# Performance work log

Hardware: AMD Instinct MI355X
Metric: run time of the kernel (lower is better)

The kernel has to match this reference:

```python
import jax, jax.numpy as jnp
import numpy as np

N_NODES = 100_000
N_EDGES = 1_600_000
D_IN, D_HID, N_CLASSES = 128, 128, 40


def setup_inputs() -> dict:
    key = jax.random.key(0)
    ks = jax.random.split(key, 8)
    x = jax.random.normal(ks[0], (N_NODES, D_IN), dtype=jnp.float32)
    edge_index = jax.random.randint(ks[1], (2, N_EDGES), 0, N_NODES, dtype=jnp.int64)
    dims = [(D_IN, D_HID), (D_HID, D_HID), (D_HID, N_CLASSES)]
    inp = {"x": x, "edge_index": edge_index}
    for i, (di, do) in enumerate(dims):
        s = 1.0 / np.sqrt(di)
        inp[f"W_l{i}"] = jax.random.normal(ks[2 + 2 * i], (di, do), dtype=jnp.float32) * s
        inp[f"W_r{i}"] = jax.random.normal(ks[3 + 2 * i], (di, do), dtype=jnp.float32) * s
        inp[f"b{i}"] = jnp.zeros((do,), dtype=jnp.float32)
    return inp


def _sage_conv(x, src, dst, deg_inv, W_l, W_r, b):
    # gather messages from source nodes, mean-aggregate at target nodes
    msg = x[src]                                        # [E, d_in]
    aggr = jax.ops.segment_sum(msg, dst, num_segments=N_NODES) * deg_inv  # [N, d_in]
    return aggr @ W_l + b + x @ W_r                     # [N, d_out]


def reference(x, edge_index, W_l0, W_r0, b0, W_l1, W_r1, b1, W_l2, W_r2, b2):
    src, dst = edge_index[0], edge_index[1]
    deg = jax.ops.segment_sum(jnp.ones((N_EDGES,), x.dtype), dst, num_segments=N_NODES)
    deg_inv = (1.0 / jnp.maximum(deg, 1.0))[:, None]    # [N, 1]

    h = _sage_conv(x, src, dst, deg_inv, W_l0, W_r0, b0)
    h = jax.nn.relu(h)  # dropout p=0.3 is identity in eval mode
    h = _sage_conv(h, src, dst, deg_inv, W_l1, W_r1, b1)
    h = jax.nn.relu(h)
    h = _sage_conv(h, src, dst, deg_inv, W_l2, W_r2, b2)
    return jax.nn.log_softmax(h, axis=1)
```

## Files before the change

kernel.cpp:

```cpp
#include <hip/hip_runtime.h>
#include <math.h>

#define THREADS 256
#define BSHIFT 8
#define BSIZE 256
#define NEB 512

typedef short short8 __attribute__((ext_vector_type(8)));
typedef float f32x4 __attribute__((ext_vector_type(4)));

__device__ __forceinline__ unsigned short f2bf(float f) {
  unsigned u = __builtin_bit_cast(unsigned, f);
  return (unsigned short)((u + 0x7FFFu + ((u >> 16) & 1u)) >> 16);
}
__device__ __forceinline__ float bflo(unsigned u) {
  return __builtin_bit_cast(float, u << 16);
}
__device__ __forceinline__ float bfhi(unsigned u) {
  return __builtin_bit_cast(float, u & 0xFFFF0000u);
}
__device__ __forceinline__ unsigned pack2(float x, float y) {
  return (unsigned)f2bf(x) | ((unsigned)f2bf(y) << 16);
}

__device__ __forceinline__ void acc8(float* a, uint4 u) {
  a[0] += bflo(u.x); a[1] += bfhi(u.x);
  a[2] += bflo(u.y); a[3] += bfhi(u.y);
  a[4] += bflo(u.z); a[5] += bfhi(u.z);
  a[6] += bflo(u.w); a[7] += bfhi(u.w);
}

__device__ __forceinline__ void gemm128_body(
    const short8 xf[4], const short8 xg[4],
    const unsigned short* __restrict__ Wswz, const float* __restrict__ bias,
    unsigned short* __restrict__ outL, unsigned short* __restrict__ outR,
    int M, int lane,
    unsigned short (*lt)[16][136], int rb0) {
  int quad = lane >> 4, n16 = lane & 15;
#pragma unroll
  for (int ct = 0; ct < 8; ++ct) {
    f32x4 accA = {0.f, 0.f, 0.f, 0.f};
    f32x4 accB = {0.f, 0.f, 0.f, 0.f};
    const unsigned short* wp = Wswz + (size_t)(ct * 64 + lane) * 8;
#pragma unroll
    for (int ks = 0; ks < 4; ++ks) {
      short8 wf = *(const short8*)(wp + ks * 8192);
      accA = __builtin_amdgcn_mfma_f32_16x16x32_bf16(wf, xf[ks], accA, 0, 0, 0);
      accB = __builtin_amdgcn_mfma_f32_16x16x32_bf16(wf, xg[ks], accB, 0, 0, 0);
    }
    int ch = ct * 16 + quad * 4;
    ushort4 oA, oB;
    oA.x = f2bf(accA[0]); oA.y = f2bf(accA[1]); oA.z = f2bf(accA[2]); oA.w = f2bf(accA[3]);
    oB.x = f2bf(accB[0]); oB.y = f2bf(accB[1]); oB.z = f2bf(accB[2]); oB.w = f2bf(accB[3]);
    *(ushort4*)&lt[0][n16][ch] = oA;
    *(ushort4*)&lt[1][n16][ch] = oB;
  }
#pragma unroll
  for (int r = 0; r < 4; ++r) {
    int nd = r * 4 + (lane >> 4);
    int ic = (lane & 15) * 8;
    uint4 vA = *(const uint4*)&lt[0][nd][ic];
    uint4 vB = *(const uint4*)&lt[1][nd][ic];
    if (rb0 + nd < M)      *(uint4*)(outL + ((size_t)(rb0 + nd)) * 128 + ic) = vA;
    if (rb0 + 64 + nd < M) *(uint4*)(outL + ((size_t)(rb0 + 64 + nd)) * 128 + ic) = vB;
  }
#pragma unroll
  for (int ct = 8; ct < 16; ++ct) {
    f32x4 accA = {0.f, 0.f, 0.f, 0.f};
    f32x4 accB = {0.f, 0.f, 0.f, 0.f};
    const unsigned short* wp = Wswz + (size_t)(ct * 64 + lane) * 8;
#pragma unroll
    for (int ks = 0; ks < 4; ++ks) {
      short8 wf = *(const short8*)(wp + ks * 8192);
      accA = __builtin_amdgcn_mfma_f32_16x16x32_bf16(wf, xf[ks], accA, 0, 0, 0);
      accB = __builtin_amdgcn_mfma_f32_16x16x32_bf16(wf, xg[ks], accB, 0, 0, 0);
    }
    int ch = (ct - 8) * 16 + quad * 4;
    float4 bv = *(const float4*)(bias + ch);
    ushort4 oA, oB;
    oA.x = f2bf(accA[0] + bv.x); oA.y = f2bf(accA[1] + bv.y);
    oA.z = f2bf(accA[2] + bv.z); oA.w = f2bf(accA[3] + bv.w);
    oB.x = f2bf(accB[0] + bv.x); oB.y = f2bf(accB[1] + bv.y);
    oB.z = f2bf(accB[2] + bv.z); oB.w = f2bf(accB[3] + bv.w);
    *(ushort4*)&lt[0][n16][ch] = oA;
    *(ushort4*)&lt[1][n16][ch] = oB;
  }
#pragma unroll
  for (int r = 0; r < 4; ++r) {
    int nd = r * 4 + (lane >> 4);
    int ic = (lane & 15) * 8;
    uint4 vA = *(const uint4*)&lt[0][nd][ic];
    uint4 vB = *(const uint4*)&lt[1][nd][ic];
    if (rb0 + nd < M)      *(uint4*)(outR + ((size_t)(rb0 + nd)) * 128 + ic) = vA;
    if (rb0 + 64 + nd < M) *(uint4*)(outR + ((size_t)(rb0 + 64 + nd)) * 128 + ic) = vB;
  }
}

__global__ __launch_bounds__(256) void k_phase0(
    const int* __restrict__ dst, int* __restrict__ cnt_bm, int E, int chunk, int nbk,
    const float* __restrict__ Wl0, const float* __restrict__ Wr0,
    const float* __restrict__ Wl1, const float* __restrict__ Wr1,
    const float* __restrict__ Wl2, const float* __restrict__ Wr2,
    unsigned short* __restrict__ out0, unsigned short* __restrict__ out1,
    unsigned short* __restrict__ out2) {
  int b = blockIdx.x, t = threadIdx.x;
  if (b < NEB) {
    __shared__ int h[1024];
    for (int i = t; i < nbk; i += 256) h[i] = 0;
    __syncthreads();
    int e0 = b * chunk, e1 = min(e0 + chunk, E);
    for (int e = e0 + t; e < e1; e += 256) atomicAdd(&h[dst[e] >> BSHIFT], 1);
    __syncthreads();
    for (int i = t; i < nbk; i += 256) cnt_bm[(size_t)b * nbk + i] = h[i];
    return;
  }
  int wb = b - NEB;
  if (wb < 256) {
    const float* Wl = (wb < 128) ? Wl0 : Wl1;
    const float* Wr = (wb < 128) ? Wr0 : Wr1;
    unsigned short* out = (wb < 128) ? out0 : out1;
    int idx = (wb & 127) * 256 + t;
    int j = idx & 7, lane = (idx >> 3) & 63, ct = (idx >> 9) & 15, ks = idx >> 13;
    int k = ks * 32 + (lane >> 4) * 8 + j;
    int c = ct * 16 + (lane & 15);
    float v = (c < 128) ? Wl[k * 128 + c] : Wr[k * 128 + (c - 128)];
    out[idx] = f2bf(v);
  } else {
    int idx = (wb - 256) * 256 + t;
    int j = idx & 7, lane = (idx >> 3) & 63;
    int tile = idx >> 9;
    int ct = tile % 5, ks = tile / 5;
    int k = ks * 32 + (lane >> 4) * 8 + j;
    int c = ct * 16 + (lane & 15);
    float v = (c < 40) ? Wl2[k * 40 + c] : ((c < 80) ? Wr2[k * 40 + (c - 40)] : 0.f);
    out2[idx] = f2bf(v);
  }
}

__global__ __launch_bounds__(256) void k_phase1(
    const int* __restrict__ cnt_bm, int* __restrict__ locoff_tm,
    int* __restrict__ bktot, int nbk,
    const float* __restrict__ X, const unsigned short* __restrict__ Wswz,
    const float* __restrict__ bias,
    unsigned short* __restrict__ outL, unsigned short* __restrict__ outR, int M) {
  __shared__ int sh[256];
  __shared__ __align__(16) unsigned short lt[4][2][16][136];
  int t = threadIdx.x;
  if (blockIdx.x < (unsigned)nbk) {
    int g = blockIdx.x;
    int c0 = cnt_bm[(size_t)(2 * t) * nbk + g];
    int c1 = cnt_bm[(size_t)(2 * t + 1) * nbk + g];
    int s = c0 + c1;
    sh[t] = s;
    __syncthreads();
    for (int off = 1; off < 256; off <<= 1) {
      int v = (t >= off) ? sh[t - off] : 0;
      __syncthreads();
      if (t >= off) sh[t] += v;
      __syncthreads();
    }
    int excl = sh[t] - s;
    ((int2*)(locoff_tm + (size_t)g * NEB))[t] = make_int2(excl, excl + c0);
    if (t == 255) bktot[g] = sh[255];
    return;
  }
  int gb = blockIdx.x - nbk;
  int wave = t >> 6, lane = t & 63;
  int quad = lane >> 4, n16 = lane & 15;
  int rowA = gb * 128 + wave * 16 + n16;
  int rA = min(rowA, M - 1), rB = min(rowA + 64, M - 1);

  short8 xf[4], xg[4];
  const float* xpA = X + (size_t)rA * 128 + quad * 8;
  const float* xpB = X + (size_t)rB * 128 + quad * 8;
#pragma unroll
  for (int ks = 0; ks < 4; ++ks) {
    float4 a0 = *(const float4*)(xpA + ks * 32);
    float4 a1 = *(const float4*)(xpA + ks * 32 + 4);
    float4 b0 = *(const float4*)(xpB + ks * 32);
    float4 b1 = *(const float4*)(xpB + ks * 32 + 4);
    short8 f, g;
    f[0] = (short)f2bf(a0.x); f[1] = (short)f2bf(a0.y);
    f[2] = (short)f2bf(a0.z); f[3] = (short)f2bf(a0.w);
    f[4] = (short)f2bf(a1.x); f[5] = (short)f2bf(a1.y);
    f[6] = (short)f2bf(a1.z); f[7] = (short)f2bf(a1.w);
    g[0] = (short)f2bf(b0.x); g[1] = (short)f2bf(b0.y);
    g[2] = (short)f2bf(b0.z); g[3] = (short)f2bf(b0.w);
    g[4] = (short)f2bf(b1.x); g[5] = (short)f2bf(b1.y);
    g[6] = (short)f2bf(b1.z); g[7] = (short)f2bf(b1.w);
    xf[ks] = f;
    xg[ks] = g;
  }
  gemm128_body(xf, xg, Wswz, bias, outL, outR, M, lane,
               lt[wave], gb * 128 + wave * 16);
}

__global__ __launch_bounds__(256) void k_eplace2(
    const int* __restrict__ src, const int* __restrict__ dst,
    const int* __restrict__ bktot, const int* __restrict__ locoff_tm,
    int* __restrict__ bedge, int* __restrict__ bucket_base,
    int* __restrict__ row_ptr,
    int E, int chunk, int nbk, int N) {
  __shared__ int lptr[1024];
  __shared__ int psum[256];
  int blk = blockIdx.x, t = threadIdx.x;
  int v0 = (2 * t < nbk) ? bktot[2 * t] : 0;
  int v1 = (2 * t + 1 < nbk) ? bktot[2 * t + 1] : 0;
  int s = v0 + v1;
  psum[t] = s;
  __syncthreads();
  for (int off = 1; off < 256; off <<= 1) {
    int v = (t >= off) ? psum[t - off] : 0;
    __syncthreads();
    if (t >= off) psum[t] += v;
    __syncthreads();
  }
  int excl = psum[t] - s;
  if (2 * t < nbk)
    lptr[2 * t] = excl + locoff_tm[(size_t)(2 * t) * NEB + blk];
  if (2 * t + 1 < nbk)
    lptr[2 * t + 1] = excl + v0 + locoff_tm[(size_t)(2 * t + 1) * NEB + blk];
  if (blk == 0) {
    if (2 * t < nbk)     bucket_base[2 * t] = excl;
    if (2 * t + 1 < nbk) bucket_base[2 * t + 1] = excl + v0;
    if (t == 0) { bucket_base[nbk] = E; row_ptr[N] = E; }
  }
  __syncthreads();
  int e0 = blk * chunk, e1 = min(e0 + chunk, E);
  for (int e = e0 + t; e < e1; e += 256) {
    int d = dst[e];
    int bkt = d >> BSHIFT;
    int p = atomicAdd(&lptr[bkt], 1);
    bedge[p] = (src[e] << 8) | (d & (BSIZE - 1));
  }
}

__global__ __launch_bounds__(256) void k_bcsr2(const int* __restrict__ bedge,
                                               const int* __restrict__ bucket_base,
                                               int* __restrict__ row_ptr,
                                               int* __restrict__ col, int N) {
  int g = blockIdx.x, t = threadIdx.x;
  int beg = bucket_base[g], end = bucket_base[g + 1];
  __shared__ int deg[BSIZE];
  __shared__ int sh[BSIZE];
  __shared__ int cur[BSIZE];
  deg[t] = 0;
  __syncthreads();
  for (int i = beg + t; i < end; i += 256)
    atomicAdd(&deg[bedge[i] & (BSIZE - 1)], 1);
  __syncthreads();
  int s = deg[t];
  sh[t] = s;
  __syncthreads();
  for (int off = 1; off < 256; off <<= 1) {
    int v = (t >= off) ? sh[t - off] : 0;
    __syncthreads();
    if (t >= off) sh[t] += v;
    __syncthreads();
  }
  int ex = beg + sh[t] - s;
  int node = g * BSIZE + t;
  if (node < N) row_ptr[node] = ex;
  cur[t] = ex;
  __syncthreads();
  for (int i = beg + t; i < end; i += 256) {
    int ed = bedge[i];
    int p = atomicAdd(&cur[ed & (BSIZE - 1)], 1);
    col[p] = ed >> 8;
  }
}

__global__ __launch_bounds__(256) void gemm128_mfma(
    const unsigned short* __restrict__ Xb, const unsigned short* __restrict__ Wswz,
    const float* __restrict__ bias,
    unsigned short* __restrict__ outL, unsigned short* __restrict__ outR, int M) {
  __shared__ __align__(16) unsigned short lt[4][2][16][136];
  int wave = threadIdx.x >> 6, lane = threadIdx.x & 63;
  int quad = lane >> 4, n16 = lane & 15;
  int rowA = blockIdx.x * 128 + wave * 16 + n16;
  int rA = min(rowA, M - 1), rB = min(rowA + 64, M - 1);

  short8 xf[4], xg[4];
  const unsigned short* xpA = Xb + (size_t)rA * 128 + quad * 8;
  const unsigned short* xpB = Xb + (size_t)rB * 128 + quad * 8;
#pragma unroll
  for (int ks = 0; ks < 4; ++ks) {
    xf[ks] = *(const short8*)(xpA + ks * 32);
    xg[ks] = *(const short8*)(xpB + ks * 32);
  }
  gemm128_body(xf, xg, Wswz, bias, outL, outR, M, lane,
               lt[wave], blockIdx.x * 128 + wave * 16);
}

__global__ __launch_bounds__(256) void gemm40_mfma(
    const unsigned short* __restrict__ Xb, const unsigned short* __restrict__ Wswz,
    const float* __restrict__ bias,
    unsigned short* __restrict__ tlb, float* __restrict__ tr, int M) {
  int wave = threadIdx.x >> 6, lane = threadIdx.x & 63;
  int quad = lane >> 4, n16 = lane & 15;
  int row = blockIdx.x * 64 + wave * 16 + n16;
  int row_ld = min(row, M - 1);
  bool ok = row < M;

  short8 xf[4];
  const unsigned short* xp = Xb + (size_t)row_ld * 128 + quad * 8;
#pragma unroll
  for (int ks = 0; ks < 4; ++ks) xf[ks] = *(const short8*)(xp + ks * 32);

#pragma unroll
  for (int ct = 0; ct < 5; ++ct) {
    f32x4 acc = {0.f, 0.f, 0.f, 0.f};
    const unsigned short* wp = Wswz + (size_t)(ct * 64 + lane) * 8;
#pragma unroll
    for (int ks = 0; ks < 4; ++ks) {
      short8 wf = *(const short8*)(wp + (size_t)ks * 5 * 64 * 8);
      acc = __builtin_amdgcn_mfma_f32_16x16x32_bf16(wf, xf[ks], acc, 0, 0, 0);
    }
    int cglob = ct * 16 + quad * 4;
    if (!ok) continue;
    if (cglob < 40) {
      ushort4 o;
      o.x = f2bf(acc[0]); o.y = f2bf(acc[1]); o.z = f2bf(acc[2]); o.w = f2bf(acc[3]);
      *(ushort4*)(tlb + (size_t)row * 40 + cglob) = o;
    } else {
      int c = cglob - 40;
      float4 bv = *(const float4*)(bias + c);
      float4 o;
      o.x = acc[0] + bv.x; o.y = acc[1] + bv.y;
      o.z = acc[2] + bv.z; o.w = acc[3] + bv.w;
      *(float4*)(tr + (size_t)row * 40 + c) = o;
    }
  }
}

__global__ __launch_bounds__(256) void agg128b(
    const unsigned short* __restrict__ xl, const unsigned short* __restrict__ xr,
    const int* __restrict__ row_ptr, const int* __restrict__ col,
    unsigned short* __restrict__ h, int Nn) {
  int wave = threadIdx.x >> 6;
  int lane = threadIdx.x & 63;
  int pair = lane >> 5;
  int l32 = lane & 31;
  int n = blockIdx.x * 4 + wave;
  if (n >= Nn) return;
  int beg = row_ptr[n], end = row_ptr[n + 1];
  int deg = end - beg;
  const uint2* xlq = (const uint2*)xl;
  float a0x = 0.f, a0y = 0.f, a0z = 0.f, a0w = 0.f;
  float a1x = 0.f, a1y = 0.f, a1z = 0.f, a1w = 0.f;
  float a2x = 0.f, a2y = 0.f, a2z = 0.f, a2w = 0.f;
  float a3x = 0.f, a3y = 0.f, a3z = 0.f, a3w = 0.f;
  int e = beg + pair;
  for (int it = deg >> 3; it > 0; --it, e += 8) {
    uint2 u0 = xlq[(size_t)col[e]     * 32 + l32];
    uint2 u1 = xlq[(size_t)col[e + 2] * 32 + l32];
    uint2 u2 = xlq[(size_t)col[e + 4] * 32 + l32];
    uint2 u3 = xlq[(size_t)col[e + 6] * 32 + l32];
    a0x += bflo(u0.x); a0y += bfhi(u0.x); a0z += bflo(u0.y); a0w += bfhi(u0.y);
    a1x += bflo(u1.x); a1y += bfhi(u1.x); a1z += bflo(u1.y); a1w += bfhi(u1.y);
    a2x += bflo(u2.x); a2y += bfhi(u2.x); a2z += bflo(u2.y); a2w += bfhi(u2.y);
    a3x += bflo(u3.x); a3y += bfhi(u3.x); a3z += bflo(u3.y); a3w += bfhi(u3.y);
  }
  for (; e < end; e += 2) {
    uint2 u = xlq[(size_t)col[e] * 32 + l32];
    a0x += bflo(u.x); a0y += bfhi(u.x); a0z += bflo(u.y); a0w += bfhi(u.y);
  }
  float ax = (a0x + a1x) + (a2x + a3x);
  float ay = (a0y + a1y) + (a2y + a3y);
  float az = (a0z + a1z) + (a2z + a3z);
  float aw = (a0w + a1w) + (a2w + a3w);
  ax += __shfl_xor(ax, 32);
  ay += __shfl_xor(ay, 32);
  az += __shfl_xor(az, 32);
  aw += __shfl_xor(aw, 32);
  if (pair == 0) {
    float di = 1.0f / (float)max(deg, 1);
    uint2 r = ((const uint2*)xr)[(size_t)n * 32 + l32];
    float ox = fmaxf(fmaf(ax, di, bflo(r.x)), 0.f);
    float oy = fmaxf(fmaf(ay, di, bfhi(r.x)), 0.f);
    float oz = fmaxf(fmaf(az, di, bflo(r.y)), 0.f);
    float ow = fmaxf(fmaf(aw, di, bfhi(r.y)), 0.f);
    uint2 o;
    o.x = pack2(ox, oy);
    o.y = pack2(oz, ow);
    ((uint2*)h)[(size_t)n * 32 + l32] = o;
  }
}

__global__ __launch_bounds__(256) void agg40_lsm(
    const unsigned short* __restrict__ tlb, const float* __restrict__ tr,
    const int* __restrict__ row_ptr, const int* __restrict__ col,
    float* __restrict__ out, int Nn) {
  int wave = threadIdx.x >> 6;
  int lane = threadIdx.x & 63;
  int ew = lane >> 3;
  int l8 = lane & 7;
  int n = blockIdx.x * 4 + wave;
  if (n >= Nn) return;
  int beg = row_ptr[n], end = row_ptr[n + 1];
  int deg = end - beg;
  const uint4* tlq = (const uint4*)tlb;
  float a0[8], a1[8];
#pragma unroll
  for (int j = 0; j < 8; ++j) { a0[j] = 0.f; a1[j] = 0.f; }
  int rounds = (deg + 15) >> 4;
  if (rounds > 0) {
    int end1 = end - 1;
    int e = beg + ew;
    int c0 = col[min(e, end1)];
    int c1 = col[min(e + 8, end1)];
    for (int it = rounds - 1; it > 0; --it) {
      uint4 u0 = tlq[(size_t)c0 * 5 + l8];
      uint4 u1 = tlq[(size_t)c1 * 5 + l8];
      int en = e + 16;
      int cn0 = col[min(en, end1)];
      int cn1 = col[min(en + 8, end1)];
      acc8(a0, u0); acc8(a1, u1);
      c0 = cn0; c1 = cn1; e = en;
    }
    uint4 u0 = tlq[(size_t)c0 * 5 + l8];
    uint4 u1 = tlq[(size_t)c1 * 5 + l8];
    uint4 z = make_uint4(0u, 0u, 0u, 0u);
    if (e >= end) u0 = z;
    if (e + 8 >= end) u1 = z;
    acc8(a0, u0); acc8(a1, u1);
  }
  float v[8];
#pragma unroll
  for (int j = 0; j < 8; ++j) {
    float t = a0[j] + a1[j];
    t += __shfl_xor(t, 32);
    t += __shfl_xor(t, 16);
    t += __shfl_xor(t, 8);
    v[j] = t;
  }
  bool valid = l8 < 5;
  float di = 1.0f / (float)max(deg, 1);
  float4 r0 = valid ? *(const float4*)(tr + (size_t)n * 40 + 8 * l8)
                    : make_float4(0.f, 0.f, 0.f, 0.f);
  float4 r1 = valid ? *(const float4*)(tr + (size_t)n * 40 + 8 * l8 + 4)
                    : make_float4(0.f, 0.f, 0.f, 0.f);
  float rb[8] = {r0.x, r0.y, r0.z, r0.w, r1.x, r1.y, r1.z, r1.w};
  float vv[8];
#pragma unroll
  for (int j = 0; j < 8; ++j) vv[j] = valid ? fmaf(v[j], di, rb[j]) : -INFINITY;
  float m = vv[0];
#pragma unroll
  for (int j = 1; j < 8; ++j) m = fmaxf(m, vv[j]);
#pragma unroll
  for (int off = 4; off; off >>= 1) m = fmaxf(m, __shfl_xor(m, off));
  float ex = 0.f;
  if (valid) {
#pragma unroll
    for (int j = 0; j < 8; ++j) ex += expf(vv[j] - m);
  }
  float ssum = ex;
#pragma unroll
  for (int off = 4; off; off >>= 1) ssum += __shfl_xor(ssum, off);
  float lg = logf(ssum);
  if (ew == 0 && valid) {
    float4 o0, o1;
    o0.x = (vv[0] - m) - lg; o0.y = (vv[1] - m) - lg;
    o0.z = (vv[2] - m) - lg; o0.w = (vv[3] - m) - lg;
    o1.x = (vv[4] - m) - lg; o1.y = (vv[5] - m) - lg;
    o1.z = (vv[6] - m) - lg; o1.w = (vv[7] - m) - lg;
    *(float4*)(out + (size_t)n * 40 + 8 * l8) = o0;
    *(float4*)(out + (size_t)n * 40 + 8 * l8 + 4) = o1;
  }
}


extern "C" void kernel_launch(void* const* d_in, const int* in_sizes, int n_in,
                              void* d_out, int out_size, void* d_ws, size_t ws_size,
                              hipStream_t stream) {
  const float* x   = (const float*)d_in[0];
  const int*   ei  = (const int*)d_in[1];
  const float* Wl0 = (const float*)d_in[2];
  const float* Wr0 = (const float*)d_in[3];
  const float* b0  = (const float*)d_in[4];
  const float* Wl1 = (const float*)d_in[5];
  const float* Wr1 = (const float*)d_in[6];
  const float* b1  = (const float*)d_in[7];
  const float* Wl2 = (const float*)d_in[8];
  const float* Wr2 = (const float*)d_in[9];
  const float* b2  = (const float*)d_in[10];

  int N = in_sizes[0] / 128;
  int E = in_sizes[1] / 2;
  const int* src = ei;
  const int* dst = ei + E;
  int nbk = (N + BSIZE - 1) / BSIZE;
  int chunk = (E + NEB - 1) / NEB;

  char* ws = (char*)d_ws;
  size_t off = 0;
  auto alloc = [&](size_t bytes) -> void* {
    void* p = ws + off;
    off += (bytes + 255) & ~(size_t)255;
    return p;
  };
  unsigned short* gA  = (unsigned short*)alloc((size_t)N * 128 * 2);
  unsigned short* gB  = (unsigned short*)alloc((size_t)N * 128 * 2);
  unsigned short* hC  = (unsigned short*)alloc((size_t)N * 128 * 2);
  unsigned short* tlb = (unsigned short*)alloc((size_t)N * 40 * 2);
  float* tr           = (float*)alloc((size_t)N * 40 * 4);
  int* row_ptr  = (int*)alloc((size_t)(N + 1) * 4);
  int* col      = (int*)alloc((size_t)E * 4);
  int* bedge    = (int*)alloc((size_t)E * 4);
  int* cnt_bm   = (int*)alloc((size_t)NEB * nbk * 4);
  int* locoff   = (int*)alloc((size_t)nbk * NEB * 4);
  int* bktot    = (int*)alloc((size_t)nbk * 4);
  int* bbase    = (int*)alloc((size_t)(nbk + 1) * 4);
  unsigned short* wswz0 = (unsigned short*)alloc(32768 * 2);
  unsigned short* wswz1 = (unsigned short*)alloc(32768 * 2);
  unsigned short* wswz2 = (unsigned short*)alloc(10240 * 2);
  (void)ws_size; (void)n_in; (void)out_size;

  int gg128 = (N + 127) / 128;
  int gg = (N + 63) / 64;
  int nb = (N + 3) / 4;

  k_phase0<<<NEB + 296, 256, 0, stream>>>(dst, cnt_bm, E, chunk, nbk,
                                          Wl0, Wr0, Wl1, Wr1, Wl2, Wr2,
                                          wswz0, wswz1, wswz2);
  k_phase1<<<nbk + gg128, 256, 0, stream>>>(cnt_bm, locoff, bktot, nbk,
                                            x, wswz0, b0, gA, gB, N);
  k_eplace2<<<NEB, 256, 0, stream>>>(src, dst, bktot, locoff, bedge, bbase,
                                     row_ptr, E, chunk, nbk, N);
  k_bcsr2<<<nbk, 256, 0, stream>>>(bedge, bbase, row_ptr, col, N);

  agg128b<<<nb, 256, 0, stream>>>(gA, gB, row_ptr, col, hC, N);
  gemm128_mfma<<<gg128, 256, 0, stream>>>(hC, wswz1, b1, gA, gB, N);
  agg128b<<<nb, 256, 0, stream>>>(gA, gB, row_ptr, col, hC, N);
  gemm40_mfma<<<gg, 256, 0, stream>>>(hC, wswz2, b2, tlb, tr, N);
  agg40_lsm<<<nb, 256, 0, stream>>>(tlb, tr, row_ptr, col, (float*)d_out, N);
}
```

Measured before the change: 400.2 us.

## Fuse neighbor aggregation with following MFMA GEMM via shared-memory staging

Merges each 128-wide aggregation kernel with the next layer's GEMM. A block aggregates 128 (or 64) nodes into LDS, synchronizes, then runs the MFMA GEMM straight from LDS. This removes the hC intermediate write and re-read and cuts two kernel launches. The cost is that the GEMM waves sit idle behind a block barrier while aggregation finishes, and aggregation now runs as 8 or 4 waves per block covering 16 nodes each sequentially, which may reduce latency hiding for the irregular gathers. Buffers are double-buffered (gA2/gB2) and tlb/tr alias gA.

```diff
diff --git a/kernel.cpp b/kernel.cpp
--- a/kernel.cpp
+++ b/kernel.cpp
@@ -28,6 +28,53 @@
   a[2] += bflo(u.y); a[3] += bfhi(u.y);
   a[4] += bflo(u.z); a[5] += bfhi(u.z);
   a[6] += bflo(u.w); a[7] += bfhi(u.w);
+}
+
+__device__ __forceinline__ void agg_node(
+    const uint2* __restrict__ xlq, const unsigned short* __restrict__ xr,
+    const int* __restrict__ row_ptr, const int* __restrict__ col,
+    int n, int pair, int l32, unsigned short* abrow) {
+  int beg = row_ptr[n], end = row_ptr[n + 1];
+  int deg = end - beg;
+  float a0x = 0.f, a0y = 0.f, a0z = 0.f, a0w = 0.f;
+  float a1x = 0.f, a1y = 0.f, a1z = 0.f, a1w = 0.f;
+  float a2x = 0.f, a2y = 0.f, a2z = 0.f, a2w = 0.f;
+  float a3x = 0.f, a3y = 0.f, a3z = 0.f, a3w = 0.f;
+  int e = beg + pair;
+  for (int it = deg >> 3; it > 0; --it, e += 8) {
+    uint2 u0 = xlq[(size_t)col[e]     * 32 + l32];
+    uint2 u1 = xlq[(size_t)col[e + 2] * 32 + l32];
+    uint2 u2 = xlq[(size_t)col[e + 4] * 32 + l32];
+    uint2 u3 = xlq[(size_t)col[e + 6] * 32 + l32];
+    a0x += bflo(u0.x); a0y += bfhi(u0.x); a0z += bflo(u0.y); a0w += bfhi(u0.y);
+    a1x += bflo(u1.x); a1y += bfhi(u1.x); a1z += bflo(u1.y); a1w += bfhi(u1.y);
+    a2x += bflo(u2.x); a2y += bfhi(u2.x); a2z += bflo(u2.y); a2w += bfhi(u2.y);
+    a3x += bflo(u3.x); a3y += bfhi(u3.x); a3z += bflo(u3.y); a3w += bfhi(u3.y);
+  }
+  for (; e < end; e += 2) {
+    uint2 u = xlq[(size_t)col[e] * 32 + l32];
+    a0x += bflo(u.x); a0y += bfhi(u.x); a0z += bflo(u.y); a0w += bfhi(u.y);
+  }
+  float ax = (a0x + a1x) + (a2x + a3x);
+  float ay = (a0y + a1y) + (a2y + a3y);
+  float az = (a0z + a1z) + (a2z + a3z);
+  float aw = (a0w + a1w) + (a2w + a3w);
+  ax += __shfl_xor(ax, 32);
+  ay += __shfl_xor(ay, 32);
+  az += __shfl_xor(az, 32);
+  aw += __shfl_xor(aw, 32);
+  if (pair == 0) {
+    float di = 1.0f / (float)max(deg, 1);
+    uint2 r = ((const uint2*)xr)[(size_t)n * 32 + l32];
+    float ox = fmaxf(fmaf(ax, di, bflo(r.x)), 0.f);
+    float oy = fmaxf(fmaf(ay, di, bfhi(r.x)), 0.f);
+    float oz = fmaxf(fmaf(az, di, bflo(r.y)), 0.f);
+    float ow = fmaxf(fmaf(aw, di, bfhi(r.y)), 0.f);
+    uint2 o;
+    o.x = pack2(ox, oy);
+    o.y = pack2(oz, ow);
+    *(uint2*)(abrow + l32 * 4) = o;
+  }
 }
 
 __device__ __forceinline__ void gemm128_body(
@@ -270,43 +317,65 @@
   }
 }
 
-__global__ __launch_bounds__(256) void gemm128_mfma(
-    const unsigned short* __restrict__ Xb, const unsigned short* __restrict__ Wswz,
-    const float* __restrict__ bias,
-    unsigned short* __restrict__ outL, unsigned short* __restrict__ outR, int M) {
+__global__ __launch_bounds__(512) void k_aggemm128(
+    const unsigned short* __restrict__ xl, const unsigned short* __restrict__ xr,
+    const int* __restrict__ row_ptr, const int* __restrict__ col,
+    const unsigned short* __restrict__ Wswz, const float* __restrict__ bias,
+    unsigned short* __restrict__ outL, unsigned short* __restrict__ outR, int Nn) {
+  __shared__ __align__(16) unsigned short ab[128][132];
   __shared__ __align__(16) unsigned short lt[4][2][16][136];
   int wave = threadIdx.x >> 6, lane = threadIdx.x & 63;
+  int pair = lane >> 5, l32 = lane & 31;
+  int nb0 = blockIdx.x * 128;
+  const uint2* xlq = (const uint2*)xl;
+#pragma unroll 1
+  for (int i = 0; i < 16; ++i) {
+    int nl = wave * 16 + i;
+    int n = nb0 + nl;
+    if (n >= Nn) break;
+    agg_node(xlq, xr, row_ptr, col, n, pair, l32, &ab[nl][0]);
+  }
+  __syncthreads();
+  if (wave < 4) {
+    int quad = lane >> 4, n16 = lane & 15;
+    int rowAl = wave * 16 + n16;
+    short8 xf[4], xg[4];
+#pragma unroll
+    for (int ks = 0; ks < 4; ++ks) {
+      xf[ks] = *(const short8*)&ab[rowAl][quad * 8 + ks * 32];
+      xg[ks] = *(const short8*)&ab[rowAl + 64][quad * 8 + ks * 32];
+    }
+    gemm128_body(xf, xg, Wswz, bias, outL, outR, Nn, lane,
+                 lt[wave], nb0 + wave * 16);
+  }
+}
+
+__global__ __launch_bounds__(256) void k_aggemm40(
+    const unsigned short* __restrict__ xl, const unsigned short* __restrict__ xr,
+    const int* __restrict__ row_ptr, const int* __restrict__ col,
+    const unsigned short* __restrict__ Wswz, const float* __restrict__ bias,
+    unsigned short* __restrict__ tlb, float* __restrict__ tr, int Nn) {
+  __shared__ __align__(16) unsigned short ab[64][132];
+  int wave = threadIdx.x >> 6, lane = threadIdx.x & 63;
+  int pair = lane >> 5, l32 = lane & 31;
+  int nb0 = blockIdx.x * 64;
+  const uint2* xlq = (const uint2*)xl;
+#pragma unroll 1
+  for (int i = 0; i < 16; ++i) {
+    int nl = wave * 16 + i;
+    int n = nb0 + nl;
+    if (n >= Nn) break;
+    agg_node(xlq, xr, row_ptr, col, n, pair, l32, &ab[nl][0]);
+  }
+  __syncthreads();
   int quad = lane >> 4, n16 = lane & 15;
-  int rowA = blockIdx.x * 128 + wave * 16 + n16;
-  int rA = min(rowA, M - 1), rB = min(rowA + 64, M - 1);
-
-  short8 xf[4], xg[4];
-  const unsigned short* xpA = Xb + (size_t)rA * 128 + quad * 8;
-  const unsigned short* xpB = Xb + (size_t)rB * 128 + quad * 8;
-#pragma unroll
-  for (int ks = 0; ks < 4; ++ks) {
-    xf[ks] = *(const short8*)(xpA + ks * 32);
-    xg[ks] = *(const short8*)(xpB + ks * 32);
-  }
-  gemm128_body(xf, xg, Wswz, bias, outL, outR, M, lane,
-               lt[wave], blockIdx.x * 128 + wave * 16);
-}
-
-__global__ __launch_bounds__(256) void gemm40_mfma(
-    const unsigned short* __restrict__ Xb, const unsigned short* __restrict__ Wswz,
-    const float* __restrict__ bias,
-    unsigned short* __restrict__ tlb, float* __restrict__ tr, int M) {
-  int wave = threadIdx.x >> 6, lane = threadIdx.x & 63;
-  int quad = lane >> 4, n16 = lane & 15;
-  int row = blockIdx.x * 64 + wave * 16 + n16;
-  int row_ld = min(row, M - 1);
-  bool ok = row < M;
-
+  int rl = wave * 16 + n16;
+  int row = nb0 + rl;
+  bool ok = row < Nn;
   short8 xf[4];
-  const unsigned short* xp = Xb + (size_t)row_ld * 128 + quad * 8;
-#pragma unroll
-  for (int ks = 0; ks < 4; ++ks) xf[ks] = *(const short8*)(xp + ks * 32);
-
+#pragma unroll
+  for (int ks = 0; ks < 4; ++ks)
+    xf[ks] = *(const short8*)&ab[rl][quad * 8 + ks * 32];
 #pragma unroll
   for (int ct = 0; ct < 5; ++ct) {
     f32x4 acc = {0.f, 0.f, 0.f, 0.f};
@@ -330,60 +399,6 @@
       o.z = acc[2] + bv.z; o.w = acc[3] + bv.w;
       *(float4*)(tr + (size_t)row * 40 + c) = o;
     }
-  }
-}
-
-__global__ __launch_bounds__(256) void agg128b(
-    const unsigned short* __restrict__ xl, const unsigned short* __restrict__ xr,
-    const int* __restrict__ row_ptr, const int* __restrict__ col,
-    unsigned short* __restrict__ h, int Nn) {
-  int wave = threadIdx.x >> 6;
-  int lane = threadIdx.x & 63;
-  int pair = lane >> 5;
-  int l32 = lane & 31;
-  int n = blockIdx.x * 4 + wave;
-  if (n >= Nn) return;
-  int beg = row_ptr[n], end = row_ptr[n + 1];
-  int deg = end - beg;
-  const uint2* xlq = (const uint2*)xl;
-  float a0x = 0.f, a0y = 0.f, a0z = 0.f, a0w = 0.f;
-  float a1x = 0.f, a1y = 0.f, a1z = 0.f, a1w = 0.f;
-  float a2x = 0.f, a2y = 0.f, a2z = 0.f, a2w = 0.f;
-  float a3x = 0.f, a3y = 0.f, a3z = 0.f, a3w = 0.f;
-  int e = beg + pair;
-  for (int it = deg >> 3; it > 0; --it, e += 8) {
-    uint2 u0 = xlq[(size_t)col[e]     * 32 + l32];
-    uint2 u1 = xlq[(size_t)col[e + 2] * 32 + l32];
-    uint2 u2 = xlq[(size_t)col[e + 4] * 32 + l32];
-    uint2 u3 = xlq[(size_t)col[e + 6] * 32 + l32];
-    a0x += bflo(u0.x); a0y += bfhi(u0.x); a0z += bflo(u0.y); a0w += bfhi(u0.y);
-    a1x += bflo(u1.x); a1y += bfhi(u1.x); a1z += bflo(u1.y); a1w += bfhi(u1.y);
-    a2x += bflo(u2.x); a2y += bfhi(u2.x); a2z += bflo(u2.y); a2w += bfhi(u2.y);
-    a3x += bflo(u3.x); a3y += bfhi(u3.x); a3z += bflo(u3.y); a3w += bfhi(u3.y);
-  }
-  for (; e < end; e += 2) {
-    uint2 u = xlq[(size_t)col[e] * 32 + l32];
-    a0x += bflo(u.x); a0y += bfhi(u.x); a0z += bflo(u.y); a0w += bfhi(u.y);
-  }
-  float ax = (a0x + a1x) + (a2x + a3x);
-  float ay = (a0y + a1y) + (a2y + a3y);
-  float az = (a0z + a1z) + (a2z + a3z);
-  float aw = (a0w + a1w) + (a2w + a3w);
-  ax += __shfl_xor(ax, 32);
-  ay += __shfl_xor(ay, 32);
-  az += __shfl_xor(az, 32);
-  aw += __shfl_xor(aw, 32);
-  if (pair == 0) {
-    float di = 1.0f / (float)max(deg, 1);
-    uint2 r = ((const uint2*)xr)[(size_t)n * 32 + l32];
-    float ox = fmaxf(fmaf(ax, di, bflo(r.x)), 0.f);
-    float oy = fmaxf(fmaf(ay, di, bfhi(r.x)), 0.f);
-    float oz = fmaxf(fmaf(az, di, bflo(r.y)), 0.f);
-    float ow = fmaxf(fmaf(aw, di, bfhi(r.y)), 0.f);
-    uint2 o;
-    o.x = pack2(ox, oy);
-    o.y = pack2(oz, ow);
-    ((uint2*)h)[(size_t)n * 32 + l32] = o;
   }
 }
 
@@ -501,9 +516,8 @@
   };
   unsigned short* gA  = (unsigned short*)alloc((size_t)N * 128 * 2);
   unsigned short* gB  = (unsigned short*)alloc((size_t)N * 128 * 2);
-  unsigned short* hC  = (unsigned short*)alloc((size_t)N * 128 * 2);
-  unsigned short* tlb = (unsigned short*)alloc((size_t)N * 40 * 2);
-  float* tr           = (float*)alloc((size_t)N * 40 * 4);
+  unsigned short* gA2 = (unsigned short*)alloc((size_t)N * 128 * 2);
+  unsigned short* gB2 = (unsigned short*)alloc((size_t)N * 128 * 2);
   int* row_ptr  = (int*)alloc((size_t)(N + 1) * 4);
   int* col      = (int*)alloc((size_t)E * 4);
   int* bedge    = (int*)alloc((size_t)E * 4);
@@ -514,10 +528,11 @@
   unsigned short* wswz0 = (unsigned short*)alloc(32768 * 2);
   unsigned short* wswz1 = (unsigned short*)alloc(32768 * 2);
   unsigned short* wswz2 = (unsigned short*)alloc(10240 * 2);
+  unsigned short* tlb = gA;
+  float* tr = (float*)((char*)gA + (((size_t)N * 40 * 2 + 255) & ~(size_t)255));
   (void)ws_size; (void)n_in; (void)out_size;
 
   int gg128 = (N + 127) / 128;
-  int gg = (N + 63) / 64;
   int nb = (N + 3) / 4;
 
   k_phase0<<<NEB + 296, 256, 0, stream>>>(dst, cnt_bm, E, chunk, nbk,
@@ -529,9 +544,9 @@
                                      row_ptr, E, chunk, nbk, N);
   k_bcsr2<<<nbk, 256, 0, stream>>>(bedge, bbase, row_ptr, col, N);
 
-  agg128b<<<nb, 256, 0, stream>>>(gA, gB, row_ptr, col, hC, N);
-  gemm128_mfma<<<gg128, 256, 0, stream>>>(hC, wswz1, b1, gA, gB, N);
-  agg128b<<<nb, 256, 0, stream>>>(gA, gB, row_ptr, col, hC, N);
-  gemm40_mfma<<<gg, 256, 0, stream>>>(hC, wswz2, b2, tlb, tr, N);
+  k_aggemm128<<<gg128, 512, 0, stream>>>(gA, gB, row_ptr, col,
+                                         wswz1, b1, gA2, gB2, N);
+  k_aggemm40<<<(N + 63) / 64, 256, 0, stream>>>(gA2, gB2, row_ptr, col,
+                                                wswz2, b2, tlb, tr, N);
   agg40_lsm<<<nb, 256, 0, stream>>>(tlb, tr, row_ptr, col, (float*)d_out, N);
 }
```

After: 443.2 us. +10.7%, slower.

## Fuse layer-2 aggregation with the 40-class GEMM through shared memory

Applied to the files above, without the earlier changes.

The second 128-wide aggregation and the final 128x80 MFMA GEMM now run in one kernel. Each block aggregates 64 nodes into a shared-memory tile and then multiplies it against the swizzled weights, so the hC round trip to global memory and one launch go away. The tlb/tr buffers now alias hC to save workspace. The LDS row padding for gemm128 also changes from 136 to 132. The cost is lower occupancy and less latency hiding, because each wave walks 16 nodes serially before the GEMM, and degree imbalance now stalls the barrier.

```diff
diff --git a/kernel.cpp b/kernel.cpp
--- a/kernel.cpp
+++ b/kernel.cpp
@@ -30,12 +30,59 @@
   a[6] += bflo(u.w); a[7] += bfhi(u.w);
 }
 
+__device__ __forceinline__ void agg_node(
+    const uint2* __restrict__ xlq, const unsigned short* __restrict__ xr,
+    const int* __restrict__ row_ptr, const int* __restrict__ col,
+    int n, int pair, int l32, unsigned short* abrow) {
+  int beg = row_ptr[n], end = row_ptr[n + 1];
+  int deg = end - beg;
+  float a0x = 0.f, a0y = 0.f, a0z = 0.f, a0w = 0.f;
+  float a1x = 0.f, a1y = 0.f, a1z = 0.f, a1w = 0.f;
+  float a2x = 0.f, a2y = 0.f, a2z = 0.f, a2w = 0.f;
+  float a3x = 0.f, a3y = 0.f, a3z = 0.f, a3w = 0.f;
+  int e = beg + pair;
+  for (int it = deg >> 3; it > 0; --it, e += 8) {
+    uint2 u0 = xlq[(size_t)col[e]     * 32 + l32];
+    uint2 u1 = xlq[(size_t)col[e + 2] * 32 + l32];
+    uint2 u2 = xlq[(size_t)col[e + 4] * 32 + l32];
+    uint2 u3 = xlq[(size_t)col[e + 6] * 32 + l32];
+    a0x += bflo(u0.x); a0y += bfhi(u0.x); a0z += bflo(u0.y); a0w += bfhi(u0.y);
+    a1x += bflo(u1.x); a1y += bfhi(u1.x); a1z += bflo(u1.y); a1w += bfhi(u1.y);
+    a2x += bflo(u2.x); a2y += bfhi(u2.x); a2z += bflo(u2.y); a2w += bfhi(u2.y);
+    a3x += bflo(u3.x); a3y += bfhi(u3.x); a3z += bflo(u3.y); a3w += bfhi(u3.y);
+  }
+  for (; e < end; e += 2) {
+    uint2 u = xlq[(size_t)col[e] * 32 + l32];
+    a0x += bflo(u.x); a0y += bfhi(u.x); a0z += bflo(u.y); a0w += bfhi(u.y);
+  }
+  float ax = (a0x + a1x) + (a2x + a3x);
+  float ay = (a0y + a1y) + (a2y + a3y);
+  float az = (a0z + a1z) + (a2z + a3z);
+  float aw = (a0w + a1w) + (a2w + a3w);
+  ax += __shfl_xor(ax, 32);
+  ay += __shfl_xor(ay, 32);
+  az += __shfl_xor(az, 32);
+  aw += __shfl_xor(aw, 32);
+  if (pair == 0) {
+    float di = 1.0f / (float)max(deg, 1);
+    uint2 r = ((const uint2*)xr)[(size_t)n * 32 + l32];
+    float ox = fmaxf(fmaf(ax, di, bflo(r.x)), 0.f);
+    float oy = fmaxf(fmaf(ay, di, bfhi(r.x)), 0.f);
+    float oz = fmaxf(fmaf(az, di, bflo(r.y)), 0.f);
+    float ow = fmaxf(fmaf(aw, di, bfhi(r.y)), 0.f);
+    uint2 o;
+    o.x = pack2(ox, oy);
+    o.y = pack2(oz, ow);
+    *(uint2*)(abrow + l32 * 4) = o;
+  }
+}
+
 __device__ __forceinline__ void gemm128_body(
     const short8 xf[4], const short8 xg[4],
     const unsigned short* __restrict__ Wswz, const float* __restrict__ bias,
     unsigned short* __restrict__ outL, unsigned short* __restrict__ outR,
     int M, int lane,
-    unsigned short (*lt)[16][136], int rb0) {
+    unsigned short (*lt)[16][132], int rb0) {
   int quad = lane >> 4, n16 = lane & 15;
 #pragma unroll
   for (int ct = 0; ct < 8; ++ct) {
@@ -144,7 +191,7 @@
     const float* __restrict__ bias,
     unsigned short* __restrict__ outL, unsigned short* __restrict__ outR, int M) {
   __shared__ int sh[256];
-  __shared__ __align__(16) unsigned short lt[4][2][16][136];
+  __shared__ __align__(16) unsigned short lt[4][2][16][132];
   int t = threadIdx.x;
   if (blockIdx.x < (unsigned)nbk) {
     int g = blockIdx.x;
@@ -267,69 +314,6 @@
     int ed = bedge[i];
     int p = atomicAdd(&cur[ed & (BSIZE - 1)], 1);
     col[p] = ed >> 8;
-  }
-}
-
-__global__ __launch_bounds__(256) void gemm128_mfma(
-    const unsigned short* __restrict__ Xb, const unsigned short* __restrict__ Wswz,
-    const float* __restrict__ bias,
-    unsigned short* __restrict__ outL, unsigned short* __restrict__ outR, int M) {
-  __shared__ __align__(16) unsigned short lt[4][2][16][136];
-  int wave = threadIdx.x >> 6, lane = threadIdx.x & 63;
-  int quad = lane >> 4, n16 = lane & 15;
-  int rowA = blockIdx.x * 128 + wave * 16 + n16;
-  int rA = min(rowA, M - 1), rB = min(rowA + 64, M - 1);
-
-  short8 xf[4], xg[4];
-  const unsigned short* xpA = Xb + (size_t)rA * 128 + quad * 8;
-  const unsigned short* xpB = Xb + (size_t)rB * 128 + quad * 8;
-#pragma unroll
-  for (int ks = 0; ks < 4; ++ks) {
-    xf[ks] = *(const short8*)(xpA + ks * 32);
-    xg[ks] = *(const short8*)(xpB + ks * 32);
-  }
-  gemm128_body(xf, xg, Wswz, bias, outL, outR, M, lane,
-               lt[wave], blockIdx.x * 128 + wave * 16);
-}
-
-__global__ __launch_bounds__(256) void gemm40_mfma(
-    const unsigned short* __restrict__ Xb, const unsigned short* __restrict__ Wswz,
-    const float* __restrict__ bias,
-    unsigned short* __restrict__ tlb, float* __restrict__ tr, int M) {
-  int wave = threadIdx.x >> 6, lane = threadIdx.x & 63;
-  int quad = lane >> 4, n16 = lane & 15;
-  int row = blockIdx.x * 64 + wave * 16 + n16;
-  int row_ld = min(row, M - 1);
-  bool ok = row < M;
-
-  short8 xf[4];
-  const unsigned short* xp = Xb + (size_t)row_ld * 128 + quad * 8;
-#pragma unroll
-  for (int ks = 0; ks < 4; ++ks) xf[ks] = *(const short8*)(xp + ks * 32);
-
-#pragma unroll
-  for (int ct = 0; ct < 5; ++ct) {
-    f32x4 acc = {0.f, 0.f, 0.f, 0.f};
-    const unsigned short* wp = Wswz + (size_t)(ct * 64 + lane) * 8;
-#pragma unroll
-    for (int ks = 0; ks < 4; ++ks) {
-      short8 wf = *(const short8*)(wp + (size_t)ks * 5 * 64 * 8);
-      acc = __builtin_amdgcn_mfma_f32_16x16x32_bf16(wf, xf[ks], acc, 0, 0, 0);
-    }
-    int cglob = ct * 16 + quad * 4;
-    if (!ok) continue;
-    if (cglob < 40) {
-      ushort4 o;
-      o.x = f2bf(acc[0]); o.y = f2bf(acc[1]); o.z = f2bf(acc[2]); o.w = f2bf(acc[3]);
-      *(ushort4*)(tlb + (size_t)row * 40 + cglob) = o;
-    } else {
-      int c = cglob - 40;
-      float4 bv = *(const float4*)(bias + c);
-      float4 o;
-      o.x = acc[0] + bv.x; o.y = acc[1] + bv.y;
-      o.z = acc[2] + bv.z; o.w = acc[3] + bv.w;
-      *(float4*)(tr + (size_t)row * 40 + c) = o;
-    }
   }
 }
 
@@ -387,6 +371,80 @@
   }
 }
 
+__global__ __launch_bounds__(256) void gemm128_mfma(
+    const unsigned short* __restrict__ Xb, const unsigned short* __restrict__ Wswz,
+    const float* __restrict__ bias,
+    unsigned short* __restrict__ outL, unsigned short* __restrict__ outR, int M) {
+  __shared__ __align__(16) unsigned short lt[4][2][16][132];
+  int wave = threadIdx.x >> 6, lane = threadIdx.x & 63;
+  int quad = lane >> 4, n16 = lane & 15;
+  int rowA = blockIdx.x * 128 + wave * 16 + n16;
+  int rA = min(rowA, M - 1), rB = min(rowA + 64, M - 1);
+
+  short8 xf[4], xg[4];
+  const unsigned short* xpA = Xb + (size_t)rA * 128 + quad * 8;
+  const unsigned short* xpB = Xb + (size_t)rB * 128 + quad * 8;
+#pragma unroll
+  for (int ks = 0; ks < 4; ++ks) {
+    xf[ks] = *(const short8*)(xpA + ks * 32);
+    xg[ks] = *(const short8*)(xpB + ks * 32);
+  }
+  gemm128_body(xf, xg, Wswz, bias, outL, outR, M, lane,
+               lt[wave], blockIdx.x * 128 + wave * 16);
+}
+
+__global__ __launch_bounds__(256) void k_aggemm40(
+    const unsigned short* __restrict__ xl, const unsigned short* __restrict__ xr,
+    const int* __restrict__ row_ptr, const int* __restrict__ col,
+    const unsigned short* __restrict__ Wswz, const float* __restrict__ bias,
+    unsigned short* __restrict__ tlb, float* __restrict__ tr, int Nn) {
+  __shared__ __align__(16) unsigned short ab[64][132];
+  int wave = threadIdx.x >> 6, lane = threadIdx.x & 63;
+  int pair = lane >> 5, l32 = lane & 31;
+  int nb0 = blockIdx.x * 64;
+  const uint2* xlq = (const uint2*)xl;
+#pragma unroll 1
+  for (int i = 0; i < 16; ++i) {
+    int nl = wave * 16 + i;
+    int n = nb0 + nl;
+    if (n >= Nn) break;
+    agg_node(xlq, xr, row_ptr, col, n, pair, l32, &ab[nl][0]);
+  }
+  __syncthreads();
+  int quad = lane >> 4, n16 = lane & 15;
+  int rl = wave * 16 + n16;
+  int row = nb0 + rl;
+  bool ok = row < Nn;
+  short8 xf[4];
+#pragma unroll
+  for (int ks = 0; ks < 4; ++ks)
+    xf[ks] = *(const short8*)&ab[rl][quad * 8 + ks * 32];
+#pragma unroll
+  for (int ct = 0; ct < 5; ++ct) {
+    f32x4 acc = {0.f, 0.f, 0.f, 0.f};
+    const unsigned short* wp = Wswz + (size_t)(ct * 64 + lane) * 8;
+#pragma unroll
+    for (int ks = 0; ks < 4; ++ks) {
+      short8 wf = *(const short8*)(wp + (size_t)ks * 5 * 64 * 8);
+      acc = __builtin_amdgcn_mfma_f32_16x16x32_bf16(wf, xf[ks], acc, 0, 0, 0);
+    }
+    int cglob = ct * 16 + quad * 4;
+    if (!ok) continue;
+    if (cglob < 40) {
+      ushort4 o;
+      o.x = f2bf(acc[0]); o.y = f2bf(acc[1]); o.z = f2bf(acc[2]); o.w = f2bf(acc[3]);
+      *(ushort4*)(tlb + (size_t)row * 40 + cglob) = o;
+    } else {
+      int c = cglob - 40;
+      float4 bv = *(const float4*)(bias + c);
+      float4 o;
+      o.x = acc[0] + bv.x; o.y = acc[1] + bv.y;
+      o.z = acc[2] + bv.z; o.w = acc[3] + bv.w;
+      *(float4*)(tr + (size_t)row * 40 + c) = o;
+    }
+  }
+}
+
 __global__ __launch_bounds__(256) void agg40_lsm(
     const unsigned short* __restrict__ tlb, const float* __restrict__ tr,
     const int* __restrict__ row_ptr, const int* __restrict__ col,
@@ -502,8 +560,6 @@
   unsigned short* gA  = (unsigned short*)alloc((size_t)N * 128 * 2);
   unsigned short* gB  = (unsigned short*)alloc((size_t)N * 128 * 2);
   unsigned short* hC  = (unsigned short*)alloc((size_t)N * 128 * 2);
-  unsigned short* tlb = (unsigned short*)alloc((size_t)N * 40 * 2);
-  float* tr           = (float*)alloc((size_t)N * 40 * 4);
   int* row_ptr  = (int*)alloc((size_t)(N + 1) * 4);
   int* col      = (int*)alloc((size_t)E * 4);
   int* bedge    = (int*)alloc((size_t)E * 4);
@@ -514,10 +570,11 @@
   unsigned short* wswz0 = (unsigned short*)alloc(32768 * 2);
   unsigned short* wswz1 = (unsigned short*)alloc(32768 * 2);
   unsigned short* wswz2 = (unsigned short*)alloc(10240 * 2);
+  unsigned short* tlb = hC;
+  float* tr = (float*)((char*)hC + (((size_t)N * 40 * 2 + 255) & ~(size_t)255));
   (void)ws_size; (void)n_in; (void)out_size;
 
   int gg128 = (N + 127) / 128;
-  int gg = (N + 63) / 64;
   int nb = (N + 3) / 4;
 
   k_phase0<<<NEB + 296, 256, 0, stream>>>(dst, cnt_bm, E, chunk, nbk,
@@ -531,7 +588,7 @@
 
   agg128b<<<nb, 256, 0, stream>>>(gA, gB, row_ptr, col, hC, N);
   gemm128_mfma<<<gg128, 256, 0, stream>>>(hC, wswz1, b1, gA, gB, N);
-  agg128b<<<nb, 256, 0, stream>>>(gA, gB, row_ptr, col, hC, N);
-  gemm40_mfma<<<gg, 256, 0, stream>>>(hC, wswz2, b2, tlb, tr, N);
+  k_aggemm40<<<(N + 63) / 64, 256, 0, stream>>>(gA, gB, row_ptr, col,
+                                                wswz2, b2, tlb, tr, N);
   agg40_lsm<<<nb, 256, 0, stream>>>(tlb, tr, row_ptr, col, (float*)d_out, N);
 }
```

Result: no change. 393.7 us (-1.6%).
